# Optimization experiments

Hardware: AMD Instinct MI355X
Metric: run time of the kernel (lower is better)

The kernel has to match this reference:

```python
import jax, jax.numpy as jnp
import numpy as np

N_NODES = 50000
N_EDGES = 800000
N_FEAT = 128
N_GRAPHS = 512
OUT_DIM = 128


def gcn_conv(x, W, b, src, dst, ew, n):
    """PyG GCNConv: h = x @ W; add self-loops (weight 1); symmetric norm
    D^-1/2 A D^-1/2 with edge weights; scatter-add messages src->dst; + bias."""
    h = x @ W  # [n, out]
    loop = jnp.arange(n)
    s = jnp.concatenate([src, loop])
    d = jnp.concatenate([dst, loop])
    w = jnp.concatenate([ew, jnp.ones((n,), x.dtype)])
    deg = jax.ops.segment_sum(w, d, num_segments=n)
    dinv = jnp.where(deg > 0, jax.lax.rsqrt(deg), 0.0)
    norm = dinv[s] * w * dinv[d]  # [E+n]
    out = jax.ops.segment_sum(h[s] * norm[:, None], d, num_segments=n)
    return out + b


def setup_inputs() -> dict:
    key = jax.random.key(0)
    ks = jax.random.split(key, 12)
    F = N_FEAT
    x = jax.random.normal(ks[0], (N_NODES, F), jnp.float32)
    edge_index = jax.random.randint(ks[1], (2, N_EDGES), 0, N_NODES, jnp.int64)
    edge_attr = jax.random.uniform(ks[2], (N_EDGES,), jnp.float32)
    # deterministic sorted graph assignment -> no empty graphs (avoids -inf in max pool)
    batch = (jnp.arange(N_NODES, dtype=jnp.int64) * N_GRAPHS) // N_NODES
    def lin(k, fi, fo):
        s = 1.0 / np.sqrt(fi)
        return jax.random.uniform(k, (fi, fo), jnp.float32, -s, s)
    return {
        "x": x, "edge_attr": edge_attr,
        "W1": lin(ks[3], F, F), "b1": jnp.zeros((F,), jnp.float32),
        "W2": lin(ks[4], F, 2 * F), "b2": jnp.zeros((2 * F,), jnp.float32),
        "W3": lin(ks[5], 2 * F, 4 * F), "b3": jnp.zeros((4 * F,), jnp.float32),
        "Wf1": lin(ks[6], 4 * F, 1024), "bf1": jnp.zeros((1024,), jnp.float32),
        "Wf2": lin(ks[7], 1024, OUT_DIM), "bf2": jnp.zeros((OUT_DIM,), jnp.float32),
        "edge_index": edge_index, "batch": batch,
    }


def reference(x, edge_attr, W1, b1, W2, b2, W3, b3, Wf1, bf1, Wf2, bf2,
              edge_index, batch):
    n = x.shape[0]
    src, dst = edge_index[0], edge_index[1]
    h = jax.nn.relu(gcn_conv(x, W1, b1, src, dst, edge_attr, n))
    h = jax.nn.relu(gcn_conv(h, W2, b2, src, dst, edge_attr, n))
    h = jax.nn.relu(gcn_conv(h, W3, b3, src, dst, edge_attr, n))
    # global max pool over nodes per graph
    g = jax.ops.segment_max(h, batch, num_segments=N_GRAPHS)  # [G, 4F]
    g = jax.nn.relu(g @ Wf1 + bf1)
    # dropout is identity in eval mode
    out = g @ Wf2 + bf2
    return out
```

## Files before the change

kernel.cpp:

```cpp
#include <hip/hip_runtime.h>

#define NNODES 50000
#define NPAD   50048
#define NEDGES 800000
#define NGRAPH 512
#define DCAP 64

typedef short bf16x8 __attribute__((ext_vector_type(8)));
typedef unsigned short u16x8 __attribute__((ext_vector_type(8)));
typedef float f32x4 __attribute__((ext_vector_type(4)));
typedef unsigned long long u64;

#define GLOAD16(g, l)                                                                 \
    __builtin_amdgcn_global_load_lds((const __attribute__((address_space(1))) unsigned*)(g), \
                                     (__attribute__((address_space(3))) unsigned*)(l), 16, 0, 0)

static __device__ __forceinline__ float b2f(unsigned short u) {
    return __uint_as_float(((unsigned)u) << 16);
}
static __device__ __forceinline__ unsigned short f2b(float f) {
    unsigned u = __float_as_uint(f);
    unsigned r = (u + 0x7fffu + ((u >> 16) & 1u)) >> 16;
    return (unsigned short)r;
}

static __device__ __forceinline__ void accum8(float (&acc)[8], float c, uint4 v) {
    unsigned w[4] = {v.x, v.y, v.z, v.w};
    #pragma unroll
    for (int i = 0; i < 4; ++i) {
        acc[2 * i]     += c * __uint_as_float(w[i] << 16);
        acc[2 * i + 1] += c * __uint_as_float(w[i] & 0xffff0000u);
    }
}

#define EBLK 782
#define TBLK 204
__global__ __launch_bounds__(256) void k_pre(const float* __restrict__ W1, const float* __restrict__ W2,
                                             const float* __restrict__ W3, const float* __restrict__ Wf1,
                                             const float* __restrict__ Wf2,
                                             unsigned short* __restrict__ T1, unsigned short* __restrict__ T2,
                                             unsigned short* __restrict__ T3, unsigned short* __restrict__ Tf1,
                                             unsigned short* __restrict__ Tf2,
                                             const int4* __restrict__ ei_s, const int4* __restrict__ ei_d,
                                             const float4* __restrict__ ew4,
                                             u64* deg_cnt, unsigned* __restrict__ edges) {
    __shared__ float sm[64][65];
    const int b = blockIdx.x;
    const int tid = threadIdx.x;
    if (b < EBLK) {
        int t = b * 256 + tid;
        if (t >= NEDGES / 4) return;
        int4 ss = ei_s[t];
        int4 dd = ei_d[t];
        float4 ww = ew4[t];
        int s[4] = {ss.x, ss.y, ss.z, ss.w};
        int d[4] = {dd.x, dd.y, dd.z, dd.w};
        float w[4] = {ww.x, ww.y, ww.z, ww.w};
        int slot[4];
        #pragma unroll
        for (int u = 0; u < 4; ++u) {
            unsigned fixed = __float2uint_rn(w[u] * 16777216.0f);
            u64 old = atomicAdd(&deg_cnt[d[u]], ((u64)1 << 32) | fixed);
            slot[u] = (int)(old >> 32);
            if (slot[u] > DCAP - 1) slot[u] = DCAP - 1;
        }
        #pragma unroll
        for (int u = 0; u < 4; ++u)
            edges[((unsigned)d[u] << 6) | slot[u]] = ((unsigned)f2b(w[u]) << 16) | (unsigned)s[u];
        return;
    }
    const int bb = b - EBLK;
    if (bb >= TBLK) return;
    const float* W; unsigned short* T; int K, N, t0;
    if (bb < 4)        { W = W1;  T = T1;  K = 128;  N = 128;  t0 = 0;   }
    else if (bb < 12)  { W = W2;  T = T2;  K = 128;  N = 256;  t0 = 4;   }
    else if (bb < 44)  { W = W3;  T = T3;  K = 256;  N = 512;  t0 = 12;  }
    else if (bb < 172) { W = Wf1; T = Tf1; K = 512;  N = 1024; t0 = 44;  }
    else               { W = Wf2; T = Tf2; K = 1024; N = 128;  t0 = 172; }
    const int tile = bb - t0;
    const int ntn = N >> 6;
    const int k0 = (tile / ntn) * 64, n0 = (tile % ntn) * 64;
    const int rr = tid >> 6, cc = tid & 63;
    #pragma unroll
    for (int r = 0; r < 16; ++r) {
        int kl = r * 4 + rr;
        sm[kl][cc] = W[(size_t)(k0 + kl) * N + n0 + cc];
    }
    __syncthreads();
    #pragma unroll
    for (int r = 0; r < 16; ++r) {
        int nl = r * 4 + rr;
        T[(size_t)(n0 + nl) * K + k0 + cc] = f2b(sm[cc][nl]);
    }
}

__global__ void k_prep(const u64* __restrict__ deg_cnt, float* __restrict__ dinv, int* __restrict__ gp) {
    int i = blockIdx.x * 256 + threadIdx.x;
    if (i < NNODES)
        dinv[i] = rsqrtf((float)(unsigned)(deg_cnt[i] & 0xffffffffull) * 5.9604645e-8f + 1.0f);
    if (i < NGRAPH * 512) gp[i] = 0;
}

template <int F, int SLICES, bool DSRC, bool EPI>
__global__ __launch_bounds__(256) void k_aggregate(const unsigned short* __restrict__ X,
                                                   const u64* __restrict__ deg_cnt,
                                                   const unsigned* __restrict__ edges,
                                                   const float* __restrict__ dinv,
                                                   unsigned short* __restrict__ Z,
                                                   const float* __restrict__ bias) {
    constexpr int FS = F / SLICES;
    constexpr int LPR = FS / 8;
    constexpr int GRP = 64 / LPR;
    constexpr int STEP = GRP * 2;
    const int bid = blockIdx.x;
    const int slice = (SLICES == 1) ? 0 : (bid & (SLICES - 1));
    const int chunk = (SLICES == 1) ? bid : (bid / SLICES);
    const int wave = threadIdx.x >> 6, lane = threadIdx.x & 63;
    const int node = chunk * 4 + wave;
    if (node >= NNODES) return;
    const int sub = lane & (LPR - 1);
    const int grp = lane / LPR;
    const int fo = slice * FS + sub * 8;
    const unsigned short* Xf = X + fo;
    const float di = dinv[node];
    const int cnt = (int)(deg_cnt[node] >> 32);
    const unsigned* erow = edges + ((unsigned)node << 6);

    const uint4 selfv = *(const uint4*)(Xf + (size_t)node * F);

    float acc[8] = {};

    const int e0 = grp;
    const int nb = (cnt + STEP - 1) / STEP;

    unsigned pa0 = 0, pb0 = 0, pa1 = 0, pb1 = 0;
    uint4 va0 = {}, vb0 = {};
    float da0 = 1.f, db0 = 1.f;
    if (nb > 0) {
        int ea = e0, eb = e0 + GRP;
        pa0 = (ea < cnt) ? erow[ea] : 0u;
        pb0 = (eb < cnt) ? erow[eb] : 0u;
        va0 = *(const uint4*)(Xf + (size_t)(pa0 & 0xffffu) * F);
        vb0 = *(const uint4*)(Xf + (size_t)(pb0 & 0xffffu) * F);
        if constexpr (DSRC) { da0 = dinv[pa0 & 0xffffu]; db0 = dinv[pb0 & 0xffffu]; }
        if (nb > 1) {
            int ea1 = e0 + STEP, eb1 = ea1 + GRP;
            pa1 = (ea1 < cnt) ? erow[ea1] : 0u;
            pb1 = (eb1 < cnt) ? erow[eb1] : 0u;
        }
    }
    for (int p = 0; p < nb; ++p) {
        uint4 va1 = {}, vb1 = {};
        float da1 = 1.f, db1 = 1.f;
        unsigned pa2 = 0, pb2 = 0;
        if (p + 1 < nb) {
            va1 = *(const uint4*)(Xf + (size_t)(pa1 & 0xffffu) * F);
            vb1 = *(const uint4*)(Xf + (size_t)(pb1 & 0xffffu) * F);
            if constexpr (DSRC) { da1 = dinv[pa1 & 0xffffu]; db1 = dinv[pb1 & 0xffffu]; }
            if (p + 2 < nb) {
                int ea = e0 + (p + 2) * STEP, eb = ea + GRP;
                pa2 = (ea < cnt) ? erow[ea] : 0u;
                pb2 = (eb < cnt) ? erow[eb] : 0u;
            }
        }
        float ca = b2f((unsigned short)(pa0 >> 16));
        float cb = b2f((unsigned short)(pb0 >> 16));
        if constexpr (DSRC) { ca *= da0; cb *= db0; }
        accum8(acc, ca, va0);
        accum8(acc, cb, vb0);
        pa0 = pa1; pb0 = pb1; va0 = va1; vb0 = vb1;
        da0 = da1; db0 = db1;
        pa1 = pa2; pb1 = pb2;
    }

    #pragma unroll
    for (int j = 0; j < 8; ++j) {
        if constexpr (GRP == 4) acc[j] += __shfl_xor(acc[j], 16, 64);
        acc[j] += __shfl_xor(acc[j], 32, 64);
    }

    if (grp == 0) {
        float bv[8];
        if constexpr (EPI) {
            float4 q0 = *(const float4*)(bias + fo);
            float4 q1 = *(const float4*)(bias + fo + 4);
            bv[0] = q0.x; bv[1] = q0.y; bv[2] = q0.z; bv[3] = q0.w;
            bv[4] = q1.x; bv[5] = q1.y; bv[6] = q1.z; bv[7] = q1.w;
        }
        const float sc = DSRC ? di : 1.0f;
        unsigned w[4] = {selfv.x, selfv.y, selfv.z, selfv.w};
        unsigned o[4];
        #pragma unroll
        for (int i = 0; i < 4; ++i) {
            float s0 = __uint_as_float(w[i] << 16);
            float s1 = __uint_as_float(w[i] & 0xffff0000u);
            float z0 = di * (acc[2 * i] + sc * s0);
            float z1 = di * (acc[2 * i + 1] + sc * s1);
            if constexpr (EPI) {
                z0 = di * fmaxf(z0 + bv[2 * i], 0.f);
                z1 = di * fmaxf(z1 + bv[2 * i + 1], 0.f);
            }
            o[i] = (unsigned)f2b(z0) | ((unsigned)f2b(z1) << 16);
        }
        uint4 ov; ov.x = o[0]; ov.y = o[1]; ov.z = o[2]; ov.w = o[3];
        *(uint4*)(Z + (size_t)node * F + fo) = ov;
    }
}

template <int CMODE>
__global__ __launch_bounds__(256) void k_gemm128(const unsigned short* __restrict__ A,
                                                 const unsigned short* __restrict__ WT,
                                                 const float* __restrict__ bias,
                                                 unsigned short* __restrict__ C,
                                                 const int* __restrict__ batch,
                                                 int* __restrict__ gp,
                                                 const float* __restrict__ rscale,
                                                 int M, int N, int K) {
    __shared__ unsigned short As[2][128 * 32];
    __shared__ unsigned short Bs[2][128 * 32];
    const int tid = threadIdx.x;

    const int nwg = gridDim.x * gridDim.y;
    const int f = blockIdx.y * gridDim.x + blockIdx.x;
    const int q = nwg >> 3, r = nwg & 7;
    const int xcd = f & 7, idx = f >> 3;
    const int w = (xcd < r) ? xcd * (q + 1) + idx : r * (q + 1) + (xcd - r) * q + idx;
    const int m0 = (w / gridDim.x) * 128;
    const int n0 = (w % gridDim.x) * 128;

    const int wave = tid >> 6, lane = tid & 63;
    const int wm = (wave >> 1) * 64, wn = (wave & 1) * 64;
    const int quad = lane >> 4, mrow = lane & 15;

    const int sr = tid >> 2;
    const int sc = (tid & 3) * 8;
    const unsigned short* Ag0 = A + (size_t)(m0 + sr) * K + sc;
    const unsigned short* Ag1 = A + (size_t)(m0 + 64 + sr) * K + sc;
    const unsigned short* Bg0 = WT + (size_t)(n0 + sr) * K + sc;
    const unsigned short* Bg1 = WT + (size_t)(n0 + 64 + sr) * K + sc;
    const int so0 = sr * 32 + sc, so1 = (64 + sr) * 32 + sc;

    f32x4 acc[4][4] = {};
    const int nsteps = K >> 5;

    GLOAD16(Ag0, &As[0][so0]);
    GLOAD16(Ag1, &As[0][so1]);
    GLOAD16(Bg0, &Bs[0][so0]);
    GLOAD16(Bg1, &Bs[0][so1]);
    __syncthreads();

    for (int step = 0; step < nsteps; ++step) {
        const int cur = step & 1;
        if (step + 1 < nsteps) {
            const int k1 = (step + 1) << 5;
            GLOAD16(Ag0 + k1, &As[cur ^ 1][so0]);
            GLOAD16(Ag1 + k1, &As[cur ^ 1][so1]);
            GLOAD16(Bg0 + k1, &Bs[cur ^ 1][so0]);
            GLOAD16(Bg1 + k1, &Bs[cur ^ 1][so1]);
        }
        bf16x8 af[4], bf[4];
        #pragma unroll
        for (int mt = 0; mt < 4; ++mt)
            af[mt] = *(const bf16x8*)&As[cur][(wm + mt * 16 + mrow) * 32 + quad * 8];
        #pragma unroll
        for (int nt = 0; nt < 4; ++nt)
            bf[nt] = *(const bf16x8*)&Bs[cur][(wn + nt * 16 + mrow) * 32 + quad * 8];
        #pragma unroll
        for (int mt = 0; mt < 4; ++mt)
            #pragma unroll
            for (int nt = 0; nt < 4; ++nt)
                acc[mt][nt] = __builtin_amdgcn_mfma_f32_16x16x32_bf16(af[mt], bf[nt], acc[mt][nt], 0, 0, 0);
        __syncthreads();
    }

    float bn[4];
    #pragma unroll
    for (int nt = 0; nt < 4; ++nt) bn[nt] = bias[n0 + wn + nt * 16 + mrow];

    if constexpr (CMODE == 0) {
        #pragma unroll
        for (int mt = 0; mt < 4; ++mt) {
            #pragma unroll
            for (int r4 = 0; r4 < 4; ++r4) {
                int row = m0 + wm + mt * 16 + quad * 4 + r4;
                if (row < M) {
                    float rs = rscale ? rscale[row] : 1.0f;
                    #pragma unroll
                    for (int nt = 0; nt < 4; ++nt) {
                        float v = fmaxf(acc[mt][nt][r4] + bn[nt], 0.f) * rs;
                        C[(size_t)row * N + n0 + wn + nt * 16 + mrow] = f2b(v);
                    }
                }
            }
        }
    } else {
        const int wr0 = m0 + wm;
        int g0i = wr0 < M ? wr0 : M - 1;
        const int g0 = batch[g0i];
        int lastr = wr0 + 63; if (lastr >= M) lastr = M - 1;
        const int gl = batch[lastr];
        bool rok[16]; int gid[16];
        #pragma unroll
        for (int mt = 0; mt < 4; ++mt)
            #pragma unroll
            for (int r4 = 0; r4 < 4; ++r4) {
                int row = wr0 + mt * 16 + quad * 4 + r4;
                rok[mt * 4 + r4] = row < M;
                gid[mt * 4 + r4] = (row < M) ? batch[row] : -1;
            }
        #pragma unroll
        for (int nt = 0; nt < 4; ++nt) {
            float v0 = 0.f, v1 = 0.f;
            #pragma unroll
            for (int mt = 0; mt < 4; ++mt)
                #pragma unroll
                for (int r4 = 0; r4 < 4; ++r4)
                    if (rok[mt * 4 + r4]) {
                        float v = fmaxf(acc[mt][nt][r4] + bn[nt], 0.f);
                        if (gid[mt * 4 + r4] == g0) v0 = fmaxf(v0, v);
                        else v1 = fmaxf(v1, v);
                    }
            v0 = fmaxf(v0, __shfl_xor(v0, 16, 64));
            v0 = fmaxf(v0, __shfl_xor(v0, 32, 64));
            v1 = fmaxf(v1, __shfl_xor(v1, 16, 64));
            v1 = fmaxf(v1, __shfl_xor(v1, 32, 64));
            if (quad == 0) {
                int c = n0 + wn + nt * 16 + mrow;
                atomicMax(&gp[(size_t)g0 * N + c], __float_as_int(v0));
                if (gl != g0) atomicMax(&gp[(size_t)gl * N + c], __float_as_int(v1));
            }
        }
    }
}

template <int CMODE, int AFP>
__global__ __launch_bounds__(256) void k_gemm_mfma(const void* __restrict__ Av,
                                                   const unsigned short* __restrict__ WT,
                                                   const float* __restrict__ bias,
                                                   void* __restrict__ Cv,
                                                   int M, int N, int K) {
    constexpr int LDK = 40;
    __shared__ unsigned short As[64 * LDK];
    __shared__ unsigned short Bs[128 * LDK];
    const int tid = threadIdx.x;
    const int m0 = blockIdx.y * 64, n0 = blockIdx.x * 128;
    const int wave = tid >> 6, lane = tid & 63;
    const int wm = (wave >> 1) * 32;
    const int wn = (wave & 1) * 64;
    const int quad = lane >> 4, mrow = lane & 15;

    const int ar = tid >> 2;
    const int ak = (tid & 3) * 8;
    const bool arow_ok = (m0 + ar) < M;
    const size_t aoff = (size_t)(m0 + ar) * K + ak;
    const unsigned short* Bg0 = WT + (size_t)(n0 + ar) * K + ak;
    const unsigned short* Bg1 = WT + (size_t)(n0 + ar + 64) * K + ak;

    f32x4 acc[2][4] = {};

    for (int k0 = 0; k0 < K; k0 += 32) {
        u16x8 av = {};
        if (arow_ok) {
            if constexpr (AFP) {
                const float* Af = (const float*)Av + aoff + k0;
                float4 f0 = *(const float4*)Af;
                float4 f1 = *(const float4*)(Af + 4);
                av[0] = (short)f2b(f0.x); av[1] = (short)f2b(f0.y);
                av[2] = (short)f2b(f0.z); av[3] = (short)f2b(f0.w);
                av[4] = (short)f2b(f1.x); av[5] = (short)f2b(f1.y);
                av[6] = (short)f2b(f1.z); av[7] = (short)f2b(f1.w);
            } else {
                av = *(const u16x8*)((const unsigned short*)Av + aoff + k0);
            }
        }
        u16x8 bv0 = *(const u16x8*)(Bg0 + k0);
        u16x8 bv1 = *(const u16x8*)(Bg1 + k0);
        *(u16x8*)&As[ar * LDK + ak] = av;
        *(u16x8*)&Bs[ar * LDK + ak] = bv0;
        *(u16x8*)&Bs[(ar + 64) * LDK + ak] = bv1;
        __syncthreads();
        bf16x8 af[2], bf[4];
        #pragma unroll
        for (int mt = 0; mt < 2; ++mt)
            af[mt] = *(const bf16x8*)&As[(wm + mt * 16 + mrow) * LDK + quad * 8];
        #pragma unroll
        for (int nt = 0; nt < 4; ++nt)
            bf[nt] = *(const bf16x8*)&Bs[(wn + nt * 16 + mrow) * LDK + quad * 8];
        #pragma unroll
        for (int mt = 0; mt < 2; ++mt)
            #pragma unroll
            for (int nt = 0; nt < 4; ++nt)
                acc[mt][nt] = __builtin_amdgcn_mfma_f32_16x16x32_bf16(af[mt], bf[nt], acc[mt][nt], 0, 0, 0);
        __syncthreads();
    }

    float bn[4] = {0.f, 0.f, 0.f, 0.f};
    if constexpr (CMODE != 3) {
        #pragma unroll
        for (int nt = 0; nt < 4; ++nt) bn[nt] = bias[n0 + wn + nt * 16 + mrow];
    }

    if constexpr (CMODE == 0) {
        unsigned short* C = (unsigned short*)Cv;
        #pragma unroll
        for (int mt = 0; mt < 2; ++mt) {
            #pragma unroll
            for (int r = 0; r < 4; ++r) {
                int row = m0 + wm + mt * 16 + quad * 4 + r;
                if (row < M) {
                    #pragma unroll
                    for (int nt = 0; nt < 4; ++nt) {
                        float v = fmaxf(acc[mt][nt][r] + bn[nt], 0.f);
                        C[(size_t)row * N + n0 + wn + nt * 16 + mrow] = f2b(v);
                    }
                }
            }
        }
    } else if constexpr (CMODE == 1) {
        float* C = (float*)Cv;
        #pragma unroll
        for (int mt = 0; mt < 2; ++mt) {
            #pragma unroll
            for (int r = 0; r < 4; ++r) {
                int row = m0 + wm + mt * 16 + quad * 4 + r;
                if (row < M) {
                    #pragma unroll
                    for (int nt = 0; nt < 4; ++nt)
                        C[(size_t)row * N + n0 + wn + nt * 16 + mrow] = acc[mt][nt][r] + bn[nt];
                }
            }
        }
    } else {
        unsigned short* C = (unsigned short*)Cv;
        #pragma unroll
        for (int mt = 0; mt < 2; ++mt) {
            #pragma unroll
            for (int r = 0; r < 4; ++r) {
                int row = m0 + wm + mt * 16 + quad * 4 + r;
                if (row < M) {
                    #pragma unroll
                    for (int nt = 0; nt < 4; ++nt)
                        C[(size_t)row * N + n0 + wn + nt * 16 + mrow] = f2b(acc[mt][nt][r]);
                }
            }
        }
    }
}

extern "C" void kernel_launch(void* const* d_in, const int* in_sizes, int n_in,
                              void* d_out, int out_size, void* d_ws, size_t ws_size,
                              hipStream_t stream) {
    const float* x   = (const float*)d_in[0];
    const float* ew  = (const float*)d_in[1];
    const float* W1  = (const float*)d_in[2];
    const float* b1  = (const float*)d_in[3];
    const float* W2  = (const float*)d_in[4];
    const float* b2  = (const float*)d_in[5];
    const float* W3  = (const float*)d_in[6];
    const float* b3  = (const float*)d_in[7];
    const float* Wf1 = (const float*)d_in[8];
    const float* bf1 = (const float*)d_in[9];
    const float* Wf2 = (const float*)d_in[10];
    const float* bf2 = (const float*)d_in[11];
    const int* ei    = (const int*)d_in[12];
    const int* batch = (const int*)d_in[13];
    float* out = (float*)d_out;
    (void)in_sizes; (void)n_in; (void)out_size; (void)ws_size;

    char* p = (char*)d_ws;
    auto alloc = [&](size_t bytes) -> char* {
        char* r = p;
        p += (bytes + 255) & ~(size_t)255;
        return r;
    };
    u64*   deg_cnt = (u64*)alloc((size_t)NNODES * 8);
    float* dinv   = (float*)alloc((size_t)NNODES * 4);
    unsigned* edges = (unsigned*)alloc((size_t)NNODES * DCAP * 4);
    int*   gp     = (int*)  alloc((size_t)NGRAPH * 512 * 4);
    unsigned short* f1   = (unsigned short*)alloc((size_t)NGRAPH * 1024 * 2);
    unsigned short* wt1  = (unsigned short*)alloc((size_t)128 * 128 * 2);
    unsigned short* wt2  = (unsigned short*)alloc((size_t)256 * 128 * 2);
    unsigned short* wt3  = (unsigned short*)alloc((size_t)512 * 256 * 2);
    unsigned short* wtf1 = (unsigned short*)alloc((size_t)1024 * 512 * 2);
    unsigned short* wtf2 = (unsigned short*)alloc((size_t)128 * 1024 * 2);
    unsigned short* bufA = (unsigned short*)alloc((size_t)NPAD * 256 * 2);
    unsigned short* bufB = (unsigned short*)alloc((size_t)NPAD * 256 * 2);
    unsigned short* P1   = bufB;

    const int MB128 = (NNODES + 127) / 128;
    const int MB64  = (NNODES + 63) / 64;
    const int AGG = (NNODES + 3) / 4;

    hipMemsetAsync(deg_cnt, 0, (size_t)NNODES * 8, stream);
    k_pre<<<EBLK + TBLK, 256, 0, stream>>>(W1, W2, W3, Wf1, Wf2,
                                           wt1, wt2, wt3, wtf1, wtf2,
                                           (const int4*)ei, (const int4*)(ei + NEDGES),
                                           (const float4*)ew, deg_cnt, edges);
    k_gemm_mfma<3, 1><<<dim3(1, MB64), 256, 0, stream>>>(x, wt1, nullptr, P1, NNODES, 128, 128);
    k_prep<<<1024, 256, 0, stream>>>(deg_cnt, dinv, gp);

    k_aggregate<128, 1, true, true><<<AGG, 256, 0, stream>>>(P1, deg_cnt, edges, dinv, bufA, b1);
    k_aggregate<128, 1, false, false><<<AGG, 256, 0, stream>>>(bufA, deg_cnt, edges, dinv, bufB, nullptr);
    k_gemm128<0><<<dim3(2, MB128), 256, 0, stream>>>(bufB, wt2, b2, bufA, nullptr, nullptr, dinv, NNODES, 256, 128);
    k_aggregate<256, 2, false, false><<<AGG * 2, 256, 0, stream>>>(bufA, deg_cnt, edges, dinv, bufB, nullptr);
    k_gemm128<2><<<dim3(4, MB128), 256, 0, stream>>>(bufB, wt3, b3, nullptr, batch, gp, nullptr, NNODES, 512, 256);

    k_gemm_mfma<0, 1><<<dim3(8, NGRAPH / 64), 256, 0, stream>>>(gp, wtf1, bf1, f1, NGRAPH, 1024, 512);
    k_gemm_mfma<1, 0><<<dim3(1, NGRAPH / 64), 256, 0, stream>>>(f1, wtf2, bf2, out, NGRAPH, 128, 1024);
}
```

Measured before the change: 352.1 us.

## Remove prep kernel, compute dinv inline, split-K the MLP head GEMMs

Drops the separate k_prep launch. Layer 1's aggregation now computes dinv directly from the degree accumulator and writes it back for later layers. The zeroing of the pool buffer, the fp32 FC1 output and the final output moves into extra blocks of k_pre. The two small head GEMMs become split-K kernels that atomically add fp32 partials, with the ReLU on FC1's output applied when FC2 loads its input. This cuts the launch count and raises parallelism for the small GEMMs, at the cost of float atomics and non-deterministic summation order.

```diff
diff --git a/kernel.cpp b/kernel.cpp
--- a/kernel.cpp
+++ b/kernel.cpp
@@ -22,6 +22,9 @@
     unsigned u = __float_as_uint(f);
     unsigned r = (u + 0x7fffu + ((u >> 16) & 1u)) >> 16;
     return (unsigned short)r;
+}
+static __device__ __forceinline__ float dinv_of(unsigned wsum_fixed) {
+    return rsqrtf((float)wsum_fixed * 5.9604645e-8f + 1.0f);
 }
 
 static __device__ __forceinline__ void accum8(float (&acc)[8], float c, uint4 v) {
@@ -35,6 +38,7 @@
 
 #define EBLK 782
 #define TBLK 204
+#define ZBLK 832
 __global__ __launch_bounds__(256) void k_pre(const float* __restrict__ W1, const float* __restrict__ W2,
                                              const float* __restrict__ W3, const float* __restrict__ Wf1,
                                              const float* __restrict__ Wf2,
@@ -43,7 +47,9 @@
                                              unsigned short* __restrict__ Tf2,
                                              const int4* __restrict__ ei_s, const int4* __restrict__ ei_d,
                                              const float4* __restrict__ ew4,
-                                             u64* deg_cnt, unsigned* __restrict__ edges) {
+                                             u64* deg_cnt, unsigned* __restrict__ edges,
+                                             int* __restrict__ gp, float* __restrict__ f1f32,
+                                             float* __restrict__ outp) {
     __shared__ float sm[64][65];
     const int b = blockIdx.x;
     const int tid = threadIdx.x;
@@ -69,43 +75,45 @@
             edges[((unsigned)d[u] << 6) | slot[u]] = ((unsigned)f2b(w[u]) << 16) | (unsigned)s[u];
         return;
     }
-    const int bb = b - EBLK;
-    if (bb >= TBLK) return;
-    const float* W; unsigned short* T; int K, N, t0;
-    if (bb < 4)        { W = W1;  T = T1;  K = 128;  N = 128;  t0 = 0;   }
-    else if (bb < 12)  { W = W2;  T = T2;  K = 128;  N = 256;  t0 = 4;   }
-    else if (bb < 44)  { W = W3;  T = T3;  K = 256;  N = 512;  t0 = 12;  }
-    else if (bb < 172) { W = Wf1; T = Tf1; K = 512;  N = 1024; t0 = 44;  }
-    else               { W = Wf2; T = Tf2; K = 1024; N = 128;  t0 = 172; }
-    const int tile = bb - t0;
-    const int ntn = N >> 6;
-    const int k0 = (tile / ntn) * 64, n0 = (tile % ntn) * 64;
-    const int rr = tid >> 6, cc = tid & 63;
-    #pragma unroll
-    for (int r = 0; r < 16; ++r) {
-        int kl = r * 4 + rr;
-        sm[kl][cc] = W[(size_t)(k0 + kl) * N + n0 + cc];
-    }
-    __syncthreads();
-    #pragma unroll
-    for (int r = 0; r < 16; ++r) {
-        int nl = r * 4 + rr;
-        T[(size_t)(n0 + nl) * K + k0 + cc] = f2b(sm[cc][nl]);
-    }
-}
-
-__global__ void k_prep(const u64* __restrict__ deg_cnt, float* __restrict__ dinv, int* __restrict__ gp) {
-    int i = blockIdx.x * 256 + threadIdx.x;
-    if (i < NNODES)
-        dinv[i] = rsqrtf((float)(unsigned)(deg_cnt[i] & 0xffffffffull) * 5.9604645e-8f + 1.0f);
-    if (i < NGRAPH * 512) gp[i] = 0;
+    if (b < EBLK + TBLK) {
+        const int bb = b - EBLK;
+        const float* W; unsigned short* T; int K, N, t0;
+        if (bb < 4)        { W = W1;  T = T1;  K = 128;  N = 128;  t0 = 0;   }
+        else if (bb < 12)  { W = W2;  T = T2;  K = 128;  N = 256;  t0 = 4;   }
+        else if (bb < 44)  { W = W3;  T = T3;  K = 256;  N = 512;  t0 = 12;  }
+        else if (bb < 172) { W = Wf1; T = Tf1; K = 512;  N = 1024; t0 = 44;  }
+        else               { W = Wf2; T = Tf2; K = 1024; N = 128;  t0 = 172; }
+        const int tile = bb - t0;
+        const int ntn = N >> 6;
+        const int k0 = (tile / ntn) * 64, n0 = (tile % ntn) * 64;
+        const int rr = tid >> 6, cc = tid & 63;
+        #pragma unroll
+        for (int r = 0; r < 16; ++r) {
+            int kl = r * 4 + rr;
+            sm[kl][cc] = W[(size_t)(k0 + kl) * N + n0 + cc];
+        }
+        __syncthreads();
+        #pragma unroll
+        for (int r = 0; r < 16; ++r) {
+            int nl = r * 4 + rr;
+            T[(size_t)(n0 + nl) * K + k0 + cc] = f2b(sm[cc][nl]);
+        }
+        return;
+    }
+    const int zb = b - EBLK - TBLK;
+    if (zb >= ZBLK) return;
+    const int idx = zb * 256 + tid;
+    uint4 z4 = {0u, 0u, 0u, 0u};
+    if (zb < 256)       ((uint4*)gp)[idx] = z4;
+    else if (zb < 768)  ((uint4*)f1f32)[idx - 65536] = z4;
+    else                ((uint4*)outp)[idx - 196608] = z4;
 }
 
 template <int F, int SLICES, bool DSRC, bool EPI>
 __global__ __launch_bounds__(256) void k_aggregate(const unsigned short* __restrict__ X,
                                                    const u64* __restrict__ deg_cnt,
                                                    const unsigned* __restrict__ edges,
-                                                   const float* __restrict__ dinv,
+                                                   float* __restrict__ dinv,
                                                    unsigned short* __restrict__ Z,
                                                    const float* __restrict__ bias) {
     constexpr int FS = F / SLICES;
@@ -122,8 +130,10 @@
     const int grp = lane / LPR;
     const int fo = slice * FS + sub * 8;
     const unsigned short* Xf = X + fo;
-    const float di = dinv[node];
-    const int cnt = (int)(deg_cnt[node] >> 32);
+    const unsigned* deg_lo = (const unsigned*)deg_cnt;
+    const u64 dc = deg_cnt[node];
+    const int cnt = (int)(dc >> 32);
+    const float di = DSRC ? dinv_of((unsigned)(dc & 0xffffffffull)) : dinv[node];
     const unsigned* erow = edges + ((unsigned)node << 6);
 
     const uint4 selfv = *(const uint4*)(Xf + (size_t)node * F);
@@ -142,7 +152,10 @@
         pb0 = (eb < cnt) ? erow[eb] : 0u;
         va0 = *(const uint4*)(Xf + (size_t)(pa0 & 0xffffu) * F);
         vb0 = *(const uint4*)(Xf + (size_t)(pb0 & 0xffffu) * F);
-        if constexpr (DSRC) { da0 = dinv[pa0 & 0xffffu]; db0 = dinv[pb0 & 0xffffu]; }
+        if constexpr (DSRC) {
+            da0 = dinv_of(deg_lo[(pa0 & 0xffffu) << 1]);
+            db0 = dinv_of(deg_lo[(pb0 & 0xffffu) << 1]);
+        }
         if (nb > 1) {
             int ea1 = e0 + STEP, eb1 = ea1 + GRP;
             pa1 = (ea1 < cnt) ? erow[ea1] : 0u;
@@ -156,7 +169,10 @@
         if (p + 1 < nb) {
             va1 = *(const uint4*)(Xf + (size_t)(pa1 & 0xffffu) * F);
             vb1 = *(const uint4*)(Xf + (size_t)(pb1 & 0xffffu) * F);
-            if constexpr (DSRC) { da1 = dinv[pa1 & 0xffffu]; db1 = dinv[pb1 & 0xffffu]; }
+            if constexpr (DSRC) {
+                da1 = dinv_of(deg_lo[(pa1 & 0xffffu) << 1]);
+                db1 = dinv_of(deg_lo[(pb1 & 0xffffu) << 1]);
+            }
             if (p + 2 < nb) {
                 int ea = e0 + (p + 2) * STEP, eb = ea + GRP;
                 pa2 = (ea < cnt) ? erow[ea] : 0u;
@@ -180,6 +196,9 @@
     }
 
     if (grp == 0) {
+        if constexpr (DSRC) {
+            if (sub == 0) dinv[node] = di;
+        }
         float bv[8];
         if constexpr (EPI) {
             float4 q0 = *(const float4*)(bias + fo);
@@ -333,17 +352,18 @@
     }
 }
 
-template <int CMODE, int AFP>
+template <int CMODE, int AFP, int ARELU>
 __global__ __launch_bounds__(256) void k_gemm_mfma(const void* __restrict__ Av,
                                                    const unsigned short* __restrict__ WT,
                                                    const float* __restrict__ bias,
                                                    void* __restrict__ Cv,
-                                                   int M, int N, int K) {
+                                                   int M, int N, int K, int kchunk) {
     constexpr int LDK = 40;
     __shared__ unsigned short As[64 * LDK];
     __shared__ unsigned short Bs[128 * LDK];
     const int tid = threadIdx.x;
     const int m0 = blockIdx.y * 64, n0 = blockIdx.x * 128;
+    const int kb = blockIdx.z * kchunk, ke = kb + kchunk;
     const int wave = tid >> 6, lane = tid & 63;
     const int wm = (wave >> 1) * 32;
     const int wn = (wave & 1) * 64;
@@ -358,13 +378,19 @@
 
     f32x4 acc[2][4] = {};
 
-    for (int k0 = 0; k0 < K; k0 += 32) {
+    for (int k0 = kb; k0 < ke; k0 += 32) {
         u16x8 av = {};
         if (arow_ok) {
             if constexpr (AFP) {
                 const float* Af = (const float*)Av + aoff + k0;
                 float4 f0 = *(const float4*)Af;
                 float4 f1 = *(const float4*)(Af + 4);
+                if constexpr (ARELU) {
+                    f0.x = fmaxf(f0.x, 0.f); f0.y = fmaxf(f0.y, 0.f);
+                    f0.z = fmaxf(f0.z, 0.f); f0.w = fmaxf(f0.w, 0.f);
+                    f1.x = fmaxf(f1.x, 0.f); f1.y = fmaxf(f1.y, 0.f);
+                    f1.z = fmaxf(f1.z, 0.f); f1.w = fmaxf(f1.w, 0.f);
+                }
                 av[0] = (short)f2b(f0.x); av[1] = (short)f2b(f0.y);
                 av[2] = (short)f2b(f0.z); av[3] = (short)f2b(f0.w);
                 av[4] = (short)f2b(f1.x); av[5] = (short)f2b(f1.y);
@@ -430,7 +456,7 @@
                 }
             }
         }
-    } else {
+    } else if constexpr (CMODE == 3) {
         unsigned short* C = (unsigned short*)Cv;
         #pragma unroll
         for (int mt = 0; mt < 2; ++mt) {
@@ -441,6 +467,23 @@
                     #pragma unroll
                     for (int nt = 0; nt < 4; ++nt)
                         C[(size_t)row * N + n0 + wn + nt * 16 + mrow] = f2b(acc[mt][nt][r]);
+                }
+            }
+        }
+    } else {
+        float* C = (float*)Cv;
+        const bool addb = (kb == 0);
+        #pragma unroll
+        for (int mt = 0; mt < 2; ++mt) {
+            #pragma unroll
+            for (int r = 0; r < 4; ++r) {
+                int row = m0 + wm + mt * 16 + quad * 4 + r;
+                if (row < M) {
+                    #pragma unroll
+                    for (int nt = 0; nt < 4; ++nt) {
+                        float v = acc[mt][nt][r] + (addb ? bn[nt] : 0.f);
+                        atomicAdd(&C[(size_t)row * N + n0 + wn + nt * 16 + mrow], v);
+                    }
                 }
             }
         }
@@ -477,7 +520,7 @@
     float* dinv   = (float*)alloc((size_t)NNODES * 4);
     unsigned* edges = (unsigned*)alloc((size_t)NNODES * DCAP * 4);
     int*   gp     = (int*)  alloc((size_t)NGRAPH * 512 * 4);
-    unsigned short* f1   = (unsigned short*)alloc((size_t)NGRAPH * 1024 * 2);
+    float* f1f32  = (float*)alloc((size_t)NGRAPH * 1024 * 4);
     unsigned short* wt1  = (unsigned short*)alloc((size_t)128 * 128 * 2);
     unsigned short* wt2  = (unsigned short*)alloc((size_t)256 * 128 * 2);
     unsigned short* wt3  = (unsigned short*)alloc((size_t)512 * 256 * 2);
@@ -492,12 +535,12 @@
     const int AGG = (NNODES + 3) / 4;
 
     hipMemsetAsync(deg_cnt, 0, (size_t)NNODES * 8, stream);
-    k_pre<<<EBLK + TBLK, 256, 0, stream>>>(W1, W2, W3, Wf1, Wf2,
-                                           wt1, wt2, wt3, wtf1, wtf2,
-                                           (const int4*)ei, (const int4*)(ei + NEDGES),
-                                           (const float4*)ew, deg_cnt, edges);
-    k_gemm_mfma<3, 1><<<dim3(1, MB64), 256, 0, stream>>>(x, wt1, nullptr, P1, NNODES, 128, 128);
-    k_prep<<<1024, 256, 0, stream>>>(deg_cnt, dinv, gp);
+    k_pre<<<EBLK + TBLK + ZBLK, 256, 0, stream>>>(W1, W2, W3, Wf1, Wf2,
+                                                  wt1, wt2, wt3, wtf1, wtf2,
+                                                  (const int4*)ei, (const int4*)(ei + NEDGES),
+                                                  (const float4*)ew, deg_cnt, edges,
+                                                  gp, f1f32, out);
+    k_gemm_mfma<3, 1, 0><<<dim3(1, MB64), 256, 0, stream>>>(x, wt1, nullptr, P1, NNODES, 128, 128, 128);
 
     k_aggregate<128, 1, true, true><<<AGG, 256, 0, stream>>>(P1, deg_cnt, edges, dinv, bufA, b1);
     k_aggregate<128, 1, false, false><<<AGG, 256, 0, stream>>>(bufA, deg_cnt, edges, dinv, bufB, nullptr);
@@ -505,6 +548,6 @@
     k_aggregate<256, 2, false, false><<<AGG * 2, 256, 0, stream>>>(bufA, deg_cnt, edges, dinv, bufB, nullptr);
     k_gemm128<2><<<dim3(4, MB128), 256, 0, stream>>>(bufB, wt3, b3, nullptr, batch, gp, nullptr, NNODES, 512, 256);
 
-    k_gemm_mfma<0, 1><<<dim3(8, NGRAPH / 64), 256, 0, stream>>>(gp, wtf1, bf1, f1, NGRAPH, 1024, 512);
-    k_gemm_mfma<1, 0><<<dim3(1, NGRAPH / 64), 256, 0, stream>>>(f1, wtf2, bf2, out, NGRAPH, 128, 1024);
-}
+    k_gemm_mfma<4, 1, 0><<<dim3(8, NGRAPH / 64, 2), 256, 0, stream>>>(gp, wtf1, bf1, f1f32, NGRAPH, 1024, 512, 256);
+    k_gemm_mfma<4, 1, 1><<<dim3(1, NGRAPH / 64, 4), 256, 0, stream>>>(f1f32, wtf2, bf2, out, NGRAPH, 128, 1024, 256);
+}
```

Measured after the change: 342.2 us. -2.8%, faster.
